# Performance work log

Hardware: AMD Instinct MI355X
Metric: run time of the kernel (lower is better)

The kernel has to match this reference:

```python
import jax, jax.numpy as jnp
import numpy as np

N = 100000        # nodes
E = 1600000       # edges
NFEAT = 256
NHID = 64
NCLASS = 40
NHEADS = 4
ALPHA = 0.2       # LeakyReLU negative slope


def setup_inputs() -> dict:
    key = jax.random.key(0)
    ks = jax.random.split(key, 7)
    h = jax.random.normal(ks[0], (N, NFEAT), jnp.float32)
    src = jax.random.randint(ks[1], (E,), 0, N, dtype=jnp.int32)
    dst = jax.random.randint(ks[2], (E,), 0, N, dtype=jnp.int32)
    edge_index = jnp.stack([src, dst])  # (2, E)
    # learned parameters (xavier-ish scale)
    W_heads = jax.random.normal(ks[3], (NHEADS, NFEAT, NHID), jnp.float32) * 0.066
    a_heads = jax.random.normal(ks[4], (NHEADS, 2 * NHID, 1), jnp.float32) * 0.1
    W_out = jax.random.normal(ks[5], (NHEADS * NHID, NCLASS), jnp.float32) * 0.08
    a_out = jax.random.normal(ks[6], (2 * NCLASS, 1), jnp.float32) * 0.1
    return {"h": h, "edge_index": edge_index, "W_heads": W_heads,
            "a_heads": a_heads, "W_out": W_out, "a_out": a_out}


def gat_layer(h, src, dst, W, a, concat):
    """One GraphAttentionLayer: gather -> per-edge score -> segment softmax -> scatter."""
    Wh = h @ W                                   # (n, F_out)
    n = h.shape[0]
    F_out = Wh.shape[1]
    # a_input @ a == Wh_src @ a[:F] + Wh_dst @ a[F:], avoids (E, 2F) concat
    a_src, a_dst = a[:F_out, 0], a[F_out:, 0]
    e = jax.nn.leaky_relu(Wh[src] @ a_src + Wh[dst] @ a_dst, ALPHA)  # (E,)
    # per-destination segment softmax (stabilized; same math as exp/sum)
    m = jax.ops.segment_max(e, dst, num_segments=n)
    exp_e = jnp.exp(e - m[dst])
    denom = jax.ops.segment_sum(exp_e, dst, num_segments=n)
    att = exp_e / denom[dst]                     # (E,)
    # scatter-aggregate weighted source features
    h_prime = jax.ops.segment_sum(att[:, None] * Wh[src], dst, num_segments=n)
    return jax.nn.elu(h_prime) if concat else h_prime


def reference(h, edge_index, W_heads, a_heads, W_out, a_out):
    src, dst = edge_index[0], edge_index[1]
    # multi-head attention layers, concatenated (dropout inactive in eval)
    x = jnp.concatenate(
        [gat_layer(h, src, dst, W_heads[i], a_heads[i], True) for i in range(NHEADS)],
        axis=1)                                  # (N, NHEADS*NHID)
    x = gat_layer(x, src, dst, W_out, a_out, False)  # (N, NCLASS)
    return jax.nn.log_softmax(x, axis=1)
```

## Files before the change

### kernel.cpp

```cpp
#include <hip/hip_runtime.h>


#define ALPHA 0.2f
constexpr int N_ = 100000;
constexpr int E_ = 1600000;
constexpr long OUTEL = (long)N_ * 40;

typedef __bf16 bf16x8 __attribute__((ext_vector_type(8)));
typedef float f32x4 __attribute__((ext_vector_type(4)));

__device__ __forceinline__ unsigned short f2h(float f) {
    _Float16 h = (_Float16)f;
    return *(unsigned short*)&h;
}
__device__ __forceinline__ float h2f(unsigned short u) {
    _Float16 h = *(_Float16*)&u;
    return (float)h;
}

__global__ void k_sent(float* out, long n, float v) {
    long i = blockIdx.x * 256L + threadIdx.x;
    if (i < n) out[i] = v;
}


__global__ void k_zero(int* p, int n) {
    int i = blockIdx.x * 256 + threadIdx.x;
    if (i < n) p[i] = 0;
}

__global__ void k_count(const int* __restrict__ dst, int* __restrict__ deg) {
    int e = blockIdx.x * 256 + threadIdx.x;
    if (e < E_) {
        int d = dst[e];
        if ((unsigned)d < (unsigned)N_) atomicAdd(&deg[d], 1);
    }
}

__global__ void k_partial(const int* __restrict__ deg, int* __restrict__ part) {
    __shared__ int sd[256];
    int b = blockIdx.x, t = threadIdx.x;
    int base = b * 1024;
    int s = 0;
    for (int i = 0; i < 4; i++) {
        int idx = base + t * 4 + i;
        if (idx < N_) s += deg[idx];
    }
    sd[t] = s;
    __syncthreads();
    for (int o = 128; o; o >>= 1) {
        if (t < o) sd[t] += sd[t + o];
        __syncthreads();
    }
    if (t == 0) part[b] = sd[0];
}

__global__ void k_scan_part(int* part, int nchunks, int* rowptr) {
    __shared__ int sd[128];
    int t = threadIdx.x;
    int v = (t < nchunks) ? part[t] : 0;
    sd[t] = v;
    __syncthreads();
    for (int o = 1; o < 128; o <<= 1) {
        int add = (t >= o) ? sd[t - o] : 0;
        __syncthreads();
        sd[t] += add;
        __syncthreads();
    }
    if (t < nchunks) part[t] = sd[t] - v;
    if (t == 127) rowptr[N_] = sd[127];
}

__global__ void k_scan_final(const int* __restrict__ deg, const int* __restrict__ part,
                             int* __restrict__ rowptr, int* __restrict__ cursor) {
    __shared__ int sd[256];
    int b = blockIdx.x, t = threadIdx.x;
    int base = b * 1024;
    int v[4];
    int s = 0;
    for (int i = 0; i < 4; i++) {
        int idx = base + t * 4 + i;
        v[i] = (idx < N_) ? deg[idx] : 0;
        s += v[i];
    }
    sd[t] = s;
    __syncthreads();
    for (int o = 1; o < 256; o <<= 1) {
        int add = (t >= o) ? sd[t - o] : 0;
        __syncthreads();
        sd[t] += add;
        __syncthreads();
    }
    int off0 = part[b] + (sd[t] - s);
    for (int i = 0; i < 4; i++) {
        int idx = base + t * 4 + i;
        if (idx < N_) {
            rowptr[idx] = off0;
            cursor[idx] = off0;
            off0 += v[i];
        }
    }
}

__global__ void k_fill(const int* __restrict__ src, const int* __restrict__ dst,
                       int* __restrict__ cursor, int* __restrict__ csr) {
    int e = blockIdx.x * 256 + threadIdx.x;
    if (e < E_) {
        int d = dst[e];
        if ((unsigned)d < (unsigned)N_) {
            int p = atomicAdd(&cursor[d], 1);
            if ((unsigned)p < (unsigned)E_) csr[p] = src[e];
        }
    }
}


__global__ __launch_bounds__(320) void k_prepB(const float* __restrict__ Whd,
                                               const float* __restrict__ ah,
                                               __bf16* __restrict__ Bh, __bf16* __restrict__ Bl) {
    int k = blockIdx.x;
    int c = threadIdx.x;
    if (c >= 272) return;
    float v = 0.f;
    if (c < 256) {
        v = Whd[(c >> 6) * 16384 + k * 64 + (c & 63)];
    } else if (c < 264) {
        int hh = (c - 256) & 3;
        int isd = (c >= 260) ? 64 : 0;
        const float* wp = Whd + hh * 16384 + k * 64;
        const float* ap = ah + hh * 128 + isd;
        float s = 0.f;
        for (int j = 0; j < 64; j++) s += wp[j] * ap[j];
        v = s;
    }
    __bf16 hi = (__bf16)v;
    __bf16 lo = (__bf16)(v - (float)hi);
    size_t idx = ((size_t)(k >> 5) * 272 + c) * 32 + (k & 31);
    Bh[idx] = hi;
    Bl[idx] = lo;
}


__global__ __launch_bounds__(256) void k_gemm1m(const float* __restrict__ h,
                                                const __bf16* __restrict__ Bh,
                                                const __bf16* __restrict__ Bl,
                                                unsigned short* __restrict__ Wh1h,
                                                float* __restrict__ s1s,
                                                float* __restrict__ s1d) {
    int t = threadIdx.x;
    int wv = t >> 6, l = t & 63;
    int l15 = l & 15, lg = l >> 4;
    int rowA = blockIdx.x * 64 + wv * 16 + l15;
    bool rok = rowA < N_;
    const float* hp = h + (size_t)rowA * 256 + lg * 8;

    f32x4 acc[17];
#pragma unroll
    for (int i = 0; i < 17; i++) acc[i] = (f32x4){0.f, 0.f, 0.f, 0.f};

    for (int kc = 0; kc < 8; kc++) {
        float va[8] = {0.f, 0.f, 0.f, 0.f, 0.f, 0.f, 0.f, 0.f};
        if (rok) {
            float4 p = *(const float4*)(hp + kc * 32);
            float4 q = *(const float4*)(hp + kc * 32 + 4);
            va[0] = p.x; va[1] = p.y; va[2] = p.z; va[3] = p.w;
            va[4] = q.x; va[5] = q.y; va[6] = q.z; va[7] = q.w;
        }
        bf16x8 ahi, alo;
#pragma unroll
        for (int j = 0; j < 8; j++) {
            __bf16 hi = (__bf16)va[j];
            ahi[j] = hi;
            alo[j] = (__bf16)(va[j] - (float)hi);
        }
        const __bf16* bph = Bh + ((size_t)kc * 272 + l15) * 32 + lg * 8;
        const __bf16* bpl = Bl + ((size_t)kc * 272 + l15) * 32 + lg * 8;
#pragma unroll
        for (int tt = 0; tt < 17; tt++) {
            bf16x8 bh = *(const bf16x8*)(bph + tt * 512);
            bf16x8 bl = *(const bf16x8*)(bpl + tt * 512);
            acc[tt] = __builtin_amdgcn_mfma_f32_16x16x32_bf16(ahi, bh, acc[tt], 0, 0, 0);
            acc[tt] = __builtin_amdgcn_mfma_f32_16x16x32_bf16(alo, bh, acc[tt], 0, 0, 0);
            acc[tt] = __builtin_amdgcn_mfma_f32_16x16x32_bf16(ahi, bl, acc[tt], 0, 0, 0);
        }
    }

    int rowD0 = blockIdx.x * 64 + wv * 16 + lg * 4;
#pragma unroll
    for (int tt = 0; tt < 16; tt++) {
#pragma unroll
        for (int r = 0; r < 4; r++) {
            int orow = rowD0 + r;
            if (orow < N_) Wh1h[(size_t)orow * 256 + tt * 16 + l15] = f2h(acc[tt][r]);
        }
    }
#pragma unroll
    for (int r = 0; r < 4; r++) {
        int orow = rowD0 + r;
        if (orow < N_) {
            if (l15 < 4) s1s[orow * 4 + l15] = acc[16][r];
            else if (l15 < 8) s1d[orow * 4 + (l15 - 4)] = acc[16][r];
        }
    }
}


__global__ __launch_bounds__(256) void k_att1(const int* __restrict__ rowptr, const int* __restrict__ csr,
                                              const float* __restrict__ s1s, const float* __restrict__ s1d,
                                              float* __restrict__ att1, float* __restrict__ sinv1) {
    int t = threadIdx.x;
    int wv = t >> 6, l = t & 63;
    int n = blockIdx.x * 4 + wv;
    int base = rowptr[n], deg = rowptr[n + 1] - base;
    int i = l >> 2, hh = l & 3;
    float sdw = s1d[n * 4 + hh];

    float mx = -INFINITY;
    for (int ib = 0; ib < deg; ib += 16) {
        int e = ib + i;
        if (e < deg) {
            int s = csr[base + e];
            float v = s1s[s * 4 + hh] + sdw;
            v = v > 0.f ? v : ALPHA * v;
            mx = fmaxf(mx, v);
        }
    }
    for (int o = 4; o < 64; o <<= 1) mx = fmaxf(mx, __shfl_xor(mx, o));
    float sm = 0.f;
    for (int ib = 0; ib < deg; ib += 16) {
        int e = ib + i;
        if (e < deg) {
            int s = csr[base + e];
            float v = s1s[s * 4 + hh] + sdw;
            v = v > 0.f ? v : ALPHA * v;
            float ex = expf(v - mx);
            att1[(size_t)(base + e) * 4 + hh] = ex;
            sm += ex;
        }
    }
    for (int o = 4; o < 64; o <<= 1) sm += __shfl_xor(sm, o);
    if (l < 4) sinv1[n * 4 + hh] = (deg > 0) ? 1.f / sm : 0.f;
}


constexpr int AGG_BLOCKS = 512;
constexpr int AGG_WAVES = 16;
constexpr int NODES_PER_SWEEP = AGG_BLOCKS * AGG_WAVES;

__global__ __launch_bounds__(1024) void k_agg1g(const int* __restrict__ rowptr, const int* __restrict__ csr,
                                                const float* __restrict__ att1, const float* __restrict__ sinv1,
                                                const unsigned short* __restrict__ Wh1h,
                                                const float* __restrict__ Wo, const float* __restrict__ ao,
                                                float* __restrict__ Wh2,
                                                float* __restrict__ s2s, float* __restrict__ s2d) {
    __shared__ float WoS[256 * 40];
    __shared__ float xs[AGG_WAVES][256];
    int t = threadIdx.x;
#pragma unroll
    for (int u = 0; u < 10; u++) {
        int idx = (u * 1024 + t) * 4;
        if (idx < 256 * 40) *(float4*)(&WoS[idx]) = *(const float4*)(&Wo[idx]);
    }
    __syncthreads();

    int w = t >> 6, lane = t & 63;
    int f = lane << 2;
    int hw = lane >> 4;
    float a1 = (lane < 40) ? ao[lane] : 0.f;
    float a2 = (lane < 40) ? ao[40 + lane] : 0.f;

    for (int n = blockIdx.x * AGG_WAVES + w; n < N_; n += NODES_PER_SWEEP) {
        int base = rowptr[n], deg = rowptr[n + 1] - base;

        float4 acc = make_float4(0.f, 0.f, 0.f, 0.f);
        int i = 0;
        for (; i + 3 < deg; i += 4) {
            int b0 = base + i;
            int s0 = csr[b0], s1 = csr[b0 + 1], s2 = csr[b0 + 2], s3 = csr[b0 + 3];
            float at0 = att1[(size_t)b0 * 4 + hw];
            float at1 = att1[(size_t)(b0 + 1) * 4 + hw];
            float at2 = att1[(size_t)(b0 + 2) * 4 + hw];
            float at3 = att1[(size_t)(b0 + 3) * 4 + hw];
            ushort4 u0 = *(const ushort4*)(Wh1h + (size_t)s0 * 256 + f);
            ushort4 u1 = *(const ushort4*)(Wh1h + (size_t)s1 * 256 + f);
            ushort4 u2 = *(const ushort4*)(Wh1h + (size_t)s2 * 256 + f);
            ushort4 u3 = *(const ushort4*)(Wh1h + (size_t)s3 * 256 + f);
            acc.x += at0 * h2f(u0.x) + at1 * h2f(u1.x) + at2 * h2f(u2.x) + at3 * h2f(u3.x);
            acc.y += at0 * h2f(u0.y) + at1 * h2f(u1.y) + at2 * h2f(u2.y) + at3 * h2f(u3.y);
            acc.z += at0 * h2f(u0.z) + at1 * h2f(u1.z) + at2 * h2f(u2.z) + at3 * h2f(u3.z);
            acc.w += at0 * h2f(u0.w) + at1 * h2f(u1.w) + at2 * h2f(u2.w) + at3 * h2f(u3.w);
        }
        for (; i < deg; i++) {
            int s0 = csr[base + i];
            float at0 = att1[(size_t)(base + i) * 4 + hw];
            ushort4 u0 = *(const ushort4*)(Wh1h + (size_t)s0 * 256 + f);
            acc.x += at0 * h2f(u0.x);
            acc.y += at0 * h2f(u0.y);
            acc.z += at0 * h2f(u0.z);
            acc.w += at0 * h2f(u0.w);
        }
        float inv = sinv1[n * 4 + hw];
        acc.x *= inv; acc.y *= inv; acc.z *= inv; acc.w *= inv;
        acc.x = acc.x > 0.f ? acc.x : (expf(acc.x) - 1.f);
        acc.y = acc.y > 0.f ? acc.y : (expf(acc.y) - 1.f);
        acc.z = acc.z > 0.f ? acc.z : (expf(acc.z) - 1.f);
        acc.w = acc.w > 0.f ? acc.w : (expf(acc.w) - 1.f);
        *(float4*)(&xs[w][f]) = acc;

        float o = 0.f;
        if (lane < 40) {
            for (int k = 0; k < 256; k += 4) {
                float4 xk = *(const float4*)(&xs[w][k]);
                o += xk.x * WoS[k * 40 + lane] + xk.y * WoS[(k + 1) * 40 + lane] +
                     xk.z * WoS[(k + 2) * 40 + lane] + xk.w * WoS[(k + 3) * 40 + lane];
            }
            Wh2[(size_t)n * 40 + lane] = o;
        }
        float r1 = o * a1, r2 = o * a2;
        for (int off = 32; off; off >>= 1) {
            r1 += __shfl_xor(r1, off);
            r2 += __shfl_xor(r2, off);
        }
        if (lane == 0) {
            s2s[n] = r1;
            s2d[n] = r2;
        }
    }
}


__global__ __launch_bounds__(256) void k_l2(const int* __restrict__ rowptr, const int* __restrict__ csr,
                                            const float* __restrict__ s2s, const float* __restrict__ s2d,
                                            const float* __restrict__ Wh2, float* __restrict__ out) {
    int t = threadIdx.x;
    int wv = t >> 6, lane = t & 63;
    int n = blockIdx.x * 4 + wv;
    int base = rowptr[n], deg = rowptr[n + 1] - base;
    float sdw = s2d[n];

    float mx = -INFINITY;
    for (int i = lane; i < deg; i += 64) {
        int s = csr[base + i];
        float e = s2s[s] + sdw;
        e = e > 0.f ? e : ALPHA * e;
        mx = fmaxf(mx, e);
    }
    for (int o = 32; o; o >>= 1) mx = fmaxf(mx, __shfl_xor(mx, o));

    int e8 = lane >> 3, c8 = lane & 7;
    float acc0 = 0.f, acc1 = 0.f, acc2 = 0.f, acc3 = 0.f, acc4 = 0.f;
    float smp = 0.f;
    for (int i = e8; i < deg; i += 8) {
        int s = csr[base + i];
        float e = s2s[s] + sdw;
        e = e > 0.f ? e : ALPHA * e;
        float a = expf(e - mx);
        smp += a;
        const float* wp = Wh2 + (size_t)s * 40 + c8;
        acc0 += a * wp[0];
        acc1 += a * wp[8];
        acc2 += a * wp[16];
        acc3 += a * wp[24];
        acc4 += a * wp[32];
    }
    for (int o = 8; o < 64; o <<= 1) {
        smp += __shfl_xor(smp, o);
        acc0 += __shfl_xor(acc0, o);
        acc1 += __shfl_xor(acc1, o);
        acc2 += __shfl_xor(acc2, o);
        acc3 += __shfl_xor(acc3, o);
        acc4 += __shfl_xor(acc4, o);
    }
    float inv = (deg > 0) ? 1.f / smp : 0.f;
    acc0 *= inv; acc1 *= inv; acc2 *= inv; acc3 *= inv; acc4 *= inv;

    float mv = fmaxf(fmaxf(fmaxf(acc0, acc1), fmaxf(acc2, acc3)), acc4);
    for (int o = 1; o < 8; o <<= 1) mv = fmaxf(mv, __shfl_xor(mv, o));
    float se = expf(acc0 - mv) + expf(acc1 - mv) + expf(acc2 - mv) +
               expf(acc3 - mv) + expf(acc4 - mv);
    for (int o = 1; o < 8; o <<= 1) se += __shfl_xor(se, o);
    float lse = logf(se);
    if (e8 == 0) {
        float* op = out + (size_t)n * 40 + c8;
        op[0]  = acc0 - mv - lse;
        op[8]  = acc1 - mv - lse;
        op[16] = acc2 - mv - lse;
        op[24] = acc3 - mv - lse;
        op[32] = acc4 - mv - lse;
    }
}


extern "C" void kernel_launch(void* const* d_in, const int* in_sizes, int n_in,
                              void* d_out, int out_size, void* d_ws, size_t ws_size,
                              hipStream_t stream) {
    const float* h   = (const float*)d_in[0];
    const int*   ei  = (const int*)d_in[1];
    const float* Whd = (const float*)d_in[2];
    const float* ah  = (const float*)d_in[3];
    const float* Wo  = (const float*)d_in[4];
    const float* ao  = (const float*)d_in[5];
    float* out = (float*)d_out;

    const int* src = ei;
    const int* dst = ei + E_;
    const int nchunks = (N_ + 1023) / 1024;

    char* ws = (char*)d_ws;
    size_t off = 0;
    auto alloc = [&](size_t bytes) -> char* {
        size_t a = (off + 255) & ~(size_t)255;
        off = a + bytes;
        return ws + a;
    };
    int* rowptr = (int*)alloc((size_t)(N_ + 1) * 4);
    int* cursor = (int*)alloc((size_t)N_ * 4);
    int* deg    = (int*)alloc((size_t)N_ * 4);
    int* part   = (int*)alloc((size_t)(nchunks + 1) * 4);
    int* csr    = (int*)alloc((size_t)E_ * 4);
    float* s1s  = (float*)alloc((size_t)N_ * 4 * 4);
    float* s1d  = (float*)alloc((size_t)N_ * 4 * 4);
    float* sinv1= (float*)alloc((size_t)N_ * 4 * 4);
    float* Wh2  = (float*)alloc((size_t)N_ * 40 * 4);
    float* s2s  = (float*)alloc((size_t)N_ * 4);
    float* s2d  = (float*)alloc((size_t)N_ * 4);
    __bf16* Bh  = (__bf16*)alloc((size_t)8 * 272 * 32 * 2);
    __bf16* Bl  = (__bf16*)alloc((size_t)8 * 272 * 32 * 2);
    float* att1 = (float*)alloc((size_t)E_ * 4 * 4);
    unsigned short* Wh1h = (unsigned short*)alloc((size_t)N_ * 256 * 2);
    size_t need = off + 256;

    if (ws_size < need) {
        k_sent<<<(int)((OUTEL + 255) / 256), 256, 0, stream>>>(out, OUTEL, -2.0f);
        return;
    }

    k_prepB<<<256, 320, 0, stream>>>(Whd, ah, Bh, Bl);

    k_zero<<<(N_ + 255) / 256, 256, 0, stream>>>(deg, N_);
    k_count<<<(E_ + 255) / 256, 256, 0, stream>>>(dst, deg);
    k_partial<<<nchunks, 256, 0, stream>>>(deg, part);
    k_scan_part<<<1, 128, 0, stream>>>(part, nchunks, rowptr);
    k_scan_final<<<nchunks, 256, 0, stream>>>(deg, part, rowptr, cursor);
    k_fill<<<(E_ + 255) / 256, 256, 0, stream>>>(src, dst, cursor, csr);

    k_gemm1m<<<(N_ + 63) / 64, 256, 0, stream>>>(h, Bh, Bl, Wh1h, s1s, s1d);
    k_att1<<<N_ / 4, 256, 0, stream>>>(rowptr, csr, s1s, s1d, att1, sinv1);

    k_agg1g<<<AGG_BLOCKS, 1024, 0, stream>>>(rowptr, csr, att1, sinv1, Wh1h, Wo, ao, Wh2, s2s, s2d);

    k_l2<<<N_ / 4, 256, 0, stream>>>(rowptr, csr, s2s, s2d, Wh2, out);
}
```

Baseline: 769.9 us.

## Split layer-2 projection out of aggregation into an MFMA GEMM kernel

The fused aggregation kernel used to do a per-node 256x40 scalar matvec from LDS, plus the layer-2 attention dot products. It now only writes the ELU output x to global memory. A new MFMA GEMM kernel using a split-bf16 (hi/lo) scheme computes Wh2 together with the folded attention columns s2s and s2d. The aggregation gather is also reorganised so each half-wave handles a different edge with 8-wide fp16 loads, combined by a cross-half shuffle. This trades a 100 MB fp32 intermediate write and read, plus an extra launch, for removing the scalar LDS matvec from the gather kernel.

```diff
diff --git a/kernel.cpp b/kernel.cpp
--- a/kernel.cpp
+++ b/kernel.cpp
@@ -8,6 +8,7 @@
 
 typedef __bf16 bf16x8 __attribute__((ext_vector_type(8)));
 typedef float f32x4 __attribute__((ext_vector_type(4)));
+typedef unsigned short u16x8 __attribute__((ext_vector_type(8)));
 
 __device__ __forceinline__ unsigned short f2h(float f) {
     _Float16 h = (_Float16)f;
@@ -140,6 +141,28 @@
     Bl[idx] = lo;
 }
 
+__global__ __launch_bounds__(64) void k_prepB2(const float* __restrict__ Wo,
+                                               const float* __restrict__ ao,
+                                               __bf16* __restrict__ Boh, __bf16* __restrict__ Bol) {
+    int k = blockIdx.x;
+    int c = threadIdx.x;
+    if (c >= 48) return;
+    float v = 0.f;
+    if (c < 40) {
+        v = Wo[k * 40 + c];
+    } else if (c < 42) {
+        const float* ap = ao + (c - 40) * 40;
+        float s = 0.f;
+        for (int j = 0; j < 40; j++) s += Wo[k * 40 + j] * ap[j];
+        v = s;
+    }
+    __bf16 hi = (__bf16)v;
+    __bf16 lo = (__bf16)(v - (float)hi);
+    size_t idx = ((size_t)(k >> 5) * 48 + c) * 32 + (k & 31);
+    Boh[idx] = hi;
+    Bol[idx] = lo;
+}
+
 
 __global__ __launch_bounds__(256) void k_gemm1m(const float* __restrict__ h,
                                                 const __bf16* __restrict__ Bh,
@@ -250,80 +273,115 @@
 __global__ __launch_bounds__(1024) void k_agg1g(const int* __restrict__ rowptr, const int* __restrict__ csr,
                                                 const float* __restrict__ att1, const float* __restrict__ sinv1,
                                                 const unsigned short* __restrict__ Wh1h,
-                                                const float* __restrict__ Wo, const float* __restrict__ ao,
-                                                float* __restrict__ Wh2,
-                                                float* __restrict__ s2s, float* __restrict__ s2d) {
-    __shared__ float WoS[256 * 40];
-    __shared__ float xs[AGG_WAVES][256];
+                                                float* __restrict__ x) {
     int t = threadIdx.x;
-#pragma unroll
-    for (int u = 0; u < 10; u++) {
-        int idx = (u * 1024 + t) * 4;
-        if (idx < 256 * 40) *(float4*)(&WoS[idx]) = *(const float4*)(&Wo[idx]);
-    }
-    __syncthreads();
-
     int w = t >> 6, lane = t & 63;
-    int f = lane << 2;
-    int hw = lane >> 4;
-    float a1 = (lane < 40) ? ao[lane] : 0.f;
-    float a2 = (lane < 40) ? ao[40 + lane] : 0.f;
+    int half = lane >> 5;
+    int lh = lane & 31;
+    int f8 = lh << 3;
+    int hw = lh >> 3;
 
     for (int n = blockIdx.x * AGG_WAVES + w; n < N_; n += NODES_PER_SWEEP) {
         int base = rowptr[n], deg = rowptr[n + 1] - base;
 
-        float4 acc = make_float4(0.f, 0.f, 0.f, 0.f);
+        float acc[8] = {0.f, 0.f, 0.f, 0.f, 0.f, 0.f, 0.f, 0.f};
         int i = 0;
         for (; i + 3 < deg; i += 4) {
             int b0 = base + i;
-            int s0 = csr[b0], s1 = csr[b0 + 1], s2 = csr[b0 + 2], s3 = csr[b0 + 3];
-            float at0 = att1[(size_t)b0 * 4 + hw];
-            float at1 = att1[(size_t)(b0 + 1) * 4 + hw];
-            float at2 = att1[(size_t)(b0 + 2) * 4 + hw];
-            float at3 = att1[(size_t)(b0 + 3) * 4 + hw];
-            ushort4 u0 = *(const ushort4*)(Wh1h + (size_t)s0 * 256 + f);
-            ushort4 u1 = *(const ushort4*)(Wh1h + (size_t)s1 * 256 + f);
-            ushort4 u2 = *(const ushort4*)(Wh1h + (size_t)s2 * 256 + f);
-            ushort4 u3 = *(const ushort4*)(Wh1h + (size_t)s3 * 256 + f);
-            acc.x += at0 * h2f(u0.x) + at1 * h2f(u1.x) + at2 * h2f(u2.x) + at3 * h2f(u3.x);
-            acc.y += at0 * h2f(u0.y) + at1 * h2f(u1.y) + at2 * h2f(u2.y) + at3 * h2f(u3.y);
-            acc.z += at0 * h2f(u0.z) + at1 * h2f(u1.z) + at2 * h2f(u2.z) + at3 * h2f(u3.z);
-            acc.w += at0 * h2f(u0.w) + at1 * h2f(u1.w) + at2 * h2f(u2.w) + at3 * h2f(u3.w);
-        }
-        for (; i < deg; i++) {
-            int s0 = csr[base + i];
-            float at0 = att1[(size_t)(base + i) * 4 + hw];
-            ushort4 u0 = *(const ushort4*)(Wh1h + (size_t)s0 * 256 + f);
-            acc.x += at0 * h2f(u0.x);
-            acc.y += at0 * h2f(u0.y);
-            acc.z += at0 * h2f(u0.z);
-            acc.w += at0 * h2f(u0.w);
-        }
+            int sA = csr[b0 + half];
+            int sB = csr[b0 + 2 + half];
+            float atA = att1[(size_t)(b0 + half) * 4 + hw];
+            float atB = att1[(size_t)(b0 + 2 + half) * 4 + hw];
+            u16x8 uA = *(const u16x8*)(Wh1h + (size_t)sA * 256 + f8);
+            u16x8 uB = *(const u16x8*)(Wh1h + (size_t)sB * 256 + f8);
+#pragma unroll
+            for (int j = 0; j < 8; j++)
+                acc[j] += atA * h2f(uA[j]) + atB * h2f(uB[j]);
+        }
+        for (; i < deg; i += 2) {
+            int b0 = base + i;
+            int e = i + half;
+            bool ok = e < deg;
+            int sA = csr[b0 + (ok ? half : 0)];
+            float atA = ok ? att1[(size_t)(b0 + half) * 4 + hw] : 0.f;
+            u16x8 uA = *(const u16x8*)(Wh1h + (size_t)sA * 256 + f8);
+#pragma unroll
+            for (int j = 0; j < 8; j++)
+                acc[j] += atA * h2f(uA[j]);
+        }
+#pragma unroll
+        for (int j = 0; j < 8; j++) acc[j] += __shfl_xor(acc[j], 32);
+
         float inv = sinv1[n * 4 + hw];
-        acc.x *= inv; acc.y *= inv; acc.z *= inv; acc.w *= inv;
-        acc.x = acc.x > 0.f ? acc.x : (expf(acc.x) - 1.f);
-        acc.y = acc.y > 0.f ? acc.y : (expf(acc.y) - 1.f);
-        acc.z = acc.z > 0.f ? acc.z : (expf(acc.z) - 1.f);
-        acc.w = acc.w > 0.f ? acc.w : (expf(acc.w) - 1.f);
-        *(float4*)(&xs[w][f]) = acc;
-
-        float o = 0.f;
-        if (lane < 40) {
-            for (int k = 0; k < 256; k += 4) {
-                float4 xk = *(const float4*)(&xs[w][k]);
-                o += xk.x * WoS[k * 40 + lane] + xk.y * WoS[(k + 1) * 40 + lane] +
-                     xk.z * WoS[(k + 2) * 40 + lane] + xk.w * WoS[(k + 3) * 40 + lane];
+        int jo = half * 4;
+        float4 o;
+        o.x = acc[jo + 0] * inv; o.y = acc[jo + 1] * inv;
+        o.z = acc[jo + 2] * inv; o.w = acc[jo + 3] * inv;
+        o.x = o.x > 0.f ? o.x : (expf(o.x) - 1.f);
+        o.y = o.y > 0.f ? o.y : (expf(o.y) - 1.f);
+        o.z = o.z > 0.f ? o.z : (expf(o.z) - 1.f);
+        o.w = o.w > 0.f ? o.w : (expf(o.w) - 1.f);
+        *(float4*)(x + (size_t)n * 256 + f8 + jo) = o;
+    }
+}
+
+
+__global__ __launch_bounds__(256) void k_gemm2m(const float* __restrict__ x,
+                                                const __bf16* __restrict__ Boh,
+                                                const __bf16* __restrict__ Bol,
+                                                float* __restrict__ Wh2,
+                                                float* __restrict__ s2s,
+                                                float* __restrict__ s2d) {
+    int t = threadIdx.x;
+    int wv = t >> 6, l = t & 63;
+    int l15 = l & 15, lg = l >> 4;
+    int rowA = blockIdx.x * 64 + wv * 16 + l15;
+    bool rok = rowA < N_;
+    const float* xp = x + (size_t)rowA * 256 + lg * 8;
+
+    f32x4 acc[3];
+#pragma unroll
+    for (int i = 0; i < 3; i++) acc[i] = (f32x4){0.f, 0.f, 0.f, 0.f};
+
+    for (int kc = 0; kc < 8; kc++) {
+        float va[8] = {0.f, 0.f, 0.f, 0.f, 0.f, 0.f, 0.f, 0.f};
+        if (rok) {
+            float4 p = *(const float4*)(xp + kc * 32);
+            float4 q = *(const float4*)(xp + kc * 32 + 4);
+            va[0] = p.x; va[1] = p.y; va[2] = p.z; va[3] = p.w;
+            va[4] = q.x; va[5] = q.y; va[6] = q.z; va[7] = q.w;
+        }
+        bf16x8 ahi, alo;
+#pragma unroll
+        for (int j = 0; j < 8; j++) {
+            __bf16 hi = (__bf16)va[j];
+            ahi[j] = hi;
+            alo[j] = (__bf16)(va[j] - (float)hi);
+        }
+        const __bf16* bph = Boh + ((size_t)kc * 48 + l15) * 32 + lg * 8;
+        const __bf16* bpl = Bol + ((size_t)kc * 48 + l15) * 32 + lg * 8;
+#pragma unroll
+        for (int tt = 0; tt < 3; tt++) {
+            bf16x8 bh = *(const bf16x8*)(bph + tt * 512);
+            bf16x8 bl = *(const bf16x8*)(bpl + tt * 512);
+            acc[tt] = __builtin_amdgcn_mfma_f32_16x16x32_bf16(ahi, bh, acc[tt], 0, 0, 0);
+            acc[tt] = __builtin_amdgcn_mfma_f32_16x16x32_bf16(alo, bh, acc[tt], 0, 0, 0);
+            acc[tt] = __builtin_amdgcn_mfma_f32_16x16x32_bf16(ahi, bl, acc[tt], 0, 0, 0);
+        }
+    }
+
+    int rowD0 = blockIdx.x * 64 + wv * 16 + lg * 4;
+#pragma unroll
+    for (int tt = 0; tt < 3; tt++) {
+        int col = tt * 16 + l15;
+#pragma unroll
+        for (int r = 0; r < 4; r++) {
+            int orow = rowD0 + r;
+            if (orow < N_) {
+                if (col < 40) Wh2[(size_t)orow * 40 + col] = acc[tt][r];
+                else if (col == 40) s2s[orow] = acc[tt][r];
+                else if (col == 41) s2d[orow] = acc[tt][r];
             }
-            Wh2[(size_t)n * 40 + lane] = o;
-        }
-        float r1 = o * a1, r2 = o * a2;
-        for (int off = 32; off; off >>= 1) {
-            r1 += __shfl_xor(r1, off);
-            r2 += __shfl_xor(r2, off);
-        }
-        if (lane == 0) {
-            s2s[n] = r1;
-            s2d[n] = r2;
         }
     }
 }
@@ -426,8 +484,11 @@
     float* s2d  = (float*)alloc((size_t)N_ * 4);
     __bf16* Bh  = (__bf16*)alloc((size_t)8 * 272 * 32 * 2);
     __bf16* Bl  = (__bf16*)alloc((size_t)8 * 272 * 32 * 2);
+    __bf16* Boh = (__bf16*)alloc((size_t)8 * 48 * 32 * 2);
+    __bf16* Bol = (__bf16*)alloc((size_t)8 * 48 * 32 * 2);
     float* att1 = (float*)alloc((size_t)E_ * 4 * 4);
     unsigned short* Wh1h = (unsigned short*)alloc((size_t)N_ * 256 * 2);
+    float* x    = (float*)alloc((size_t)N_ * 256 * 4);
     size_t need = off + 256;
 
     if (ws_size < need) {
@@ -436,6 +497,7 @@
     }
 
     k_prepB<<<256, 320, 0, stream>>>(Whd, ah, Bh, Bl);
+    k_prepB2<<<256, 64, 0, stream>>>(Wo, ao, Boh, Bol);
 
     k_zero<<<(N_ + 255) / 256, 256, 0, stream>>>(deg, N_);
     k_count<<<(E_ + 255) / 256, 256, 0, stream>>>(dst, deg);
@@ -447,7 +509,9 @@
     k_gemm1m<<<(N_ + 63) / 64, 256, 0, stream>>>(h, Bh, Bl, Wh1h, s1s, s1d);
     k_att1<<<N_ / 4, 256, 0, stream>>>(rowptr, csr, s1s, s1d, att1, sinv1);
 
-    k_agg1g<<<AGG_BLOCKS, 1024, 0, stream>>>(rowptr, csr, att1, sinv1, Wh1h, Wo, ao, Wh2, s2s, s2d);
+    k_agg1g<<<AGG_BLOCKS, 1024, 0, stream>>>(rowptr, csr, att1, sinv1, Wh1h, x);
+
+    k_gemm2m<<<(N_ + 63) / 64, 256, 0, stream>>>(x, Boh, Bol, Wh2, s2s, s2d);
 
     k_l2<<<N_ / 4, 256, 0, stream>>>(rowptr, csr, s2s, s2d, Wh2, out);
 }
```

Result: faster. 728.7 us (-5.3%).
